# Kernel optimization log

Measured on AMD Instinct MI355X. Metric: run time of the kernel, lower is better.

The kernel has to match this reference:

```python
import jax, jax.numpy as jnp
import numpy as np

POWERS = (0, 1, 2)
IN_F, OUT_F = 64, 64
B, N, T = 8, 2048, 12


def setup_inputs() -> dict:
    key = jax.random.key(0)
    ks = jax.random.split(key, 8)
    inp = {
        "x": jax.random.normal(ks[0], (B, IN_F, N, T), dtype=jnp.float32),
        "adj": jax.random.uniform(ks[1], (B, N, N), dtype=jnp.float32),
    }
    # Xavier-uniform weights per adjacency power, zero biases (as in initialize_weights)
    limit = float(np.sqrt(6.0 / (IN_F + OUT_F)))
    for i, p in enumerate(POWERS):
        inp[f"W{p}"] = jax.random.uniform(ks[2 + i], (IN_F, OUT_F), jnp.float32, -limit, limit)
        inp[f"b{p}"] = jnp.zeros((OUT_F,), jnp.float32)
    return inp


def _gcn_conv(x, adj, W, b, a_power):
    # x: [B, F, N, T]; W: [F, O]; adj: [B, N, N]
    h = jnp.einsum('bfnt,fo->bont', x, W) + b[None, :, None, None]
    # repeated diffusion along node axis: h[f, n] <- sum_m adj[n, m] h[f, m]
    for _ in range(a_power):
        h = jnp.einsum('bnm,bomt->bont', adj, h)
    return jax.nn.leaky_relu(h)  # default negative_slope 0.01, same as torch


def reference(x, adj, W0, b0, W1, b1, W2, b2):
    params = {0: (W0, b0), 1: (W1, b1), 2: (W2, b2)}
    outs = [_gcn_conv(x, adj, params[p][0], params[p][1], p) for p in POWERS]
    return jnp.concatenate(outs, axis=1)  # [B, len(POWERS)*O, N, T]
```

## Files before the change

kernel.cpp:

```cpp
#include <hip/hip_runtime.h>

#define B_ 8
#define N_ 2048
#define T_ 12
#define F_ 64
#define NT 24576
#define CH 192
#define C_ 768

typedef __bf16 bf16x8 __attribute__((ext_vector_type(8)));
typedef float f32x4 __attribute__((ext_vector_type(4)));

typedef const __attribute__((address_space(1))) unsigned int as1_uint;
typedef __attribute__((address_space(3))) unsigned int as3_uint;

__device__ __forceinline__ void gload16(const void* g, void* l) {
  __builtin_amdgcn_global_load_lds((as1_uint*)g, (as3_uint*)l, 16, 0, 0);
}

__device__ __forceinline__ unsigned short f2bf(float f) {
  unsigned int u = __float_as_uint(f);
  u += 0x7FFFu + ((u >> 16) & 1u);
  return (unsigned short)(u >> 16);
}

__device__ __forceinline__ float leaky(float v) {
  return v >= 0.0f ? v : 0.01f * v;
}

__global__ __launch_bounds__(256) void convert_adj_k(const float* __restrict__ adj,
                                                     unsigned short* __restrict__ adjb) {
  size_t i = (size_t)blockIdx.x * 256 + threadIdx.x;
  const float4 v = reinterpret_cast<const float4*>(adj)[i];
  ushort4 u;
  u.x = f2bf(v.x); u.y = f2bf(v.y); u.z = f2bf(v.z); u.w = f2bf(v.w);
  reinterpret_cast<ushort4*>(adjb)[i] = u;
}

__device__ __forceinline__ void stage_wt(const float* __restrict__ W,
                                         unsigned short* Wt, int tid) {
  const int f = tid >> 2;
  const int q = tid & 3;
  const float4* row = reinterpret_cast<const float4*>(W + f * 64 + q * 16);
#pragma unroll
  for (int v4 = 0; v4 < 4; ++v4) {
    float4 v = row[v4];
    const int ob = q * 16 + v4 * 4;
    Wt[(ob + 0) * 72 + f] = f2bf(v.x);
    Wt[(ob + 1) * 72 + f] = f2bf(v.y);
    Wt[(ob + 2) * 72 + f] = f2bf(v.z);
    Wt[(ob + 3) * 72 + f] = f2bf(v.w);
  }
}

__global__ __launch_bounds__(256) void p0_k(const float* __restrict__ x,
                                            const float* __restrict__ W0,
                                            const float* __restrict__ bia0,
                                            float* __restrict__ out) {
  __shared__ unsigned short Wt[64 * 72];
  __shared__ float bias[64];
  const int tid = threadIdx.x;
  stage_wt(W0, Wt, tid);
  if (tid < 64) bias[tid] = bia0[tid];
  __syncthreads();

  const int lane = tid & 63;
  const int wave = tid >> 6;
  const int b = blockIdx.y;
  const int e = blockIdx.x * 64 + wave * 16 + (lane & 15);
  const int fgrp = (lane >> 4) * 8;
  const float* xb = x + (size_t)b * F_ * NT;

  bf16x8 xf[2];
#pragma unroll
  for (int kf = 0; kf < 2; ++kf)
#pragma unroll
    for (int j = 0; j < 8; ++j)
      xf[kf][j] = (__bf16)xb[(size_t)(fgrp + kf * 32 + j) * NT + e];

  float* outb = out + (size_t)b * CH * NT;
#pragma unroll
  for (int ob = 0; ob < 4; ++ob) {
    f32x4 acc = {};
#pragma unroll
    for (int kf = 0; kf < 2; ++kf) {
      bf16x8 af = *reinterpret_cast<const bf16x8*>(
          &Wt[(ob * 16 + (lane & 15)) * 72 + kf * 32 + fgrp]);
      acc = __builtin_amdgcn_mfma_f32_16x16x32_bf16(af, xf[kf], acc, 0, 0, 0);
    }
#pragma unroll
    for (int r = 0; r < 4; ++r) {
      const int o = ob * 16 + (lane >> 4) * 4 + r;
      outb[(size_t)o * NT + e] = leaky(acc[r] + bias[o]);
    }
  }
}

__global__ __launch_bounds__(256) void p12_k(const float* __restrict__ x,
                                             const float* __restrict__ W1,
                                             const float* __restrict__ bia1,
                                             const float* __restrict__ W2,
                                             const float* __restrict__ bia2,
                                             unsigned short* __restrict__ G1,
                                             unsigned short* __restrict__ G2) {
  __shared__ unsigned short Wt[2][64 * 72];
  __shared__ float bias[2][64];
  const int tid = threadIdx.x;
  stage_wt(W1, Wt[0], tid);
  stage_wt(W2, Wt[1], tid);
  if (tid < 64) bias[0][tid] = bia1[tid];
  else if (tid < 128) bias[1][tid - 64] = bia2[tid - 64];
  __syncthreads();

  const int lane = tid & 63;
  const int wave = tid >> 6;
  const int b = blockIdx.y;
  const int n = blockIdx.x * 16 + (lane & 15);
  const int fgrp = (lane >> 4) * 8;
  const float* xb = x + (size_t)b * F_ * NT;
  unsigned short* Gp[2] = {G1 + (size_t)b * C_ * N_, G2 + (size_t)b * C_ * N_};

#pragma unroll
  for (int it = 0; it < 3; ++it) {
    const int t = wave * 3 + it;
    const int e = n * T_ + t;

    bf16x8 xf[2];
#pragma unroll
    for (int kf = 0; kf < 2; ++kf)
#pragma unroll
      for (int j = 0; j < 8; ++j)
        xf[kf][j] = (__bf16)xb[(size_t)(fgrp + kf * 32 + j) * NT + e];

#pragma unroll
    for (int p = 0; p < 2; ++p) {
#pragma unroll
      for (int ob = 0; ob < 4; ++ob) {
        f32x4 acc = {};
#pragma unroll
        for (int kf = 0; kf < 2; ++kf) {
          bf16x8 af = *reinterpret_cast<const bf16x8*>(
              &Wt[p][(ob * 16 + (lane & 15)) * 72 + kf * 32 + fgrp]);
          acc = __builtin_amdgcn_mfma_f32_16x16x32_bf16(af, xf[kf], acc, 0, 0, 0);
        }
#pragma unroll
        for (int r = 0; r < 4; ++r) {
          const int o = ob * 16 + (lane >> 4) * 4 + r;
          Gp[p][(size_t)(o * T_ + t) * N_ + n] = f2bf(acc[r] + bias[p][o]);
        }
      }
    }
  }
}

__global__ __launch_bounds__(512, 2) void gemm8_k(
    const unsigned short* __restrict__ adjb,
    const unsigned short* __restrict__ Bt,
    float* __restrict__ out,
    unsigned short* __restrict__ Ht,
    const int mode, const int ochan_base)
{
  extern __shared__ __align__(16) unsigned short lds[];

  const int tid  = threadIdx.x;
  const int lane = tid & 63;
  const int wave = tid >> 6;
  const int wr = wave >> 2;
  const int wc = wave & 3;

  const int b  = blockIdx.x & 7;
  const int w  = blockIdx.x >> 3;
  const int n0 = (w & 7) * 256;
  const int c0 = (w >> 3) * 192;

  const unsigned short* A  = adjb + (size_t)b * N_ * N_;
  const unsigned short* Bm = Bt   + (size_t)b * C_ * N_;

  const int swzSrc = ((lane & 3) ^ ((lane >> 3) & 3)) * 8;
  const unsigned short* aSt1 = A + (size_t)(n0 + wave * 16 + (lane >> 2)) * N_ + swzSrc;
  const unsigned short* aSt2 = aSt1 + (size_t)128 * N_;
  const unsigned short* bSt1 = Bm + (size_t)(c0 + wave * 16 + (lane >> 2)) * N_ + swzSrc;
  const int brow2 = c0 + 128 + wave * 16 + (lane >> 2);
  const unsigned short* bSt2 = Bm + (size_t)(brow2 < C_ ? brow2 : C_ - 1) * N_ + swzSrc;
  const int ldsW = wave * 512;

  const int kg  = (lane >> 4) ^ ((lane >> 1) & 3);
  const int aRd = (wr * 128 + (lane & 15)) * 32 + kg * 8;
  const int bRd = (wc * 48  + (lane & 15)) * 32 + kg * 8;

  f32x4 acc[8][3] = {};
  bf16x8 afr[8], bfr[3];

#define STGA(LDSB, KT, KH) \
  gload16(aSt1 + (KT) * 64 + (KH) * 32, lds + (LDSB) + (KH) * 8192 + ldsW); \
  gload16(aSt2 + (KT) * 64 + (KH) * 32, lds + (LDSB) + (KH) * 8192 + ldsW + 4096);

#define STGB(LDSB, KT, KH) \
  gload16(bSt1 + (KT) * 64 + (KH) * 32, lds + (LDSB) + (KH) * 8192 + ldsW); \
  gload16(bSt2 + (KT) * 64 + (KH) * 32, lds + (LDSB) + (KH) * 8192 + ldsW + 4096);

#define RD_B(BUFB, KH) { \
  _Pragma("unroll") \
  for (int nf = 0; nf < 3; ++nf) \
    bfr[nf] = *(const bf16x8*)(lds + (BUFB) + (KH) * 8192 + nf * 512 + bRd); }

#define RD_A8(BUFA, KH) { \
  _Pragma("unroll") \
  for (int mm = 0; mm < 8; ++mm) \
    afr[mm] = *(const bf16x8*)(lds + (BUFA) + (KH) * 8192 + mm * 512 + aRd); }

#define MFMA24() { \
  _Pragma("unroll") \
  for (int mm = 0; mm < 8; ++mm) \
  _Pragma("unroll") \
  for (int nf = 0; nf < 3; ++nf) \
    acc[mm][nf] = __builtin_amdgcn_mfma_f32_16x16x32_bf16( \
        afr[mm], bfr[nf], acc[mm][nf], 0, 0, 0); }

#define MIDBAR() \
  __builtin_amdgcn_s_barrier(); \
  asm volatile("s_waitcnt lgkmcnt(0)" ::: "memory"); \
  __builtin_amdgcn_sched_barrier(0); \
  __builtin_amdgcn_s_setprio(1);

#define ENDBAR() \
  __builtin_amdgcn_s_setprio(0); \
  __builtin_amdgcn_s_barrier();

#define WAITV(N) asm volatile("s_waitcnt vmcnt(" #N ")" ::: "memory");

  STGA(0, 0, 0)      STGB(32768, 0, 0)
  STGA(0, 0, 1)      STGB(32768, 0, 1)
  STGA(16384, 1, 0)  STGB(49152, 1, 0)
  WAITV(8)
  __builtin_amdgcn_s_barrier();

#pragma unroll 1
  for (int it = 0; it < 15; ++it) {
    const int kt0 = 2 * it;
    RD_B(32768, 0) RD_A8(0, 0)
    STGA(16384, kt0 + 1, 1) STGB(49152, kt0 + 1, 1)
    WAITV(8)
    MIDBAR() MFMA24() ENDBAR()
    RD_B(32768, 1) RD_A8(0, 1)
    STGA(0, kt0 + 2, 0) STGB(32768, kt0 + 2, 0)
    WAITV(8)
    MIDBAR() MFMA24() ENDBAR()
    RD_B(49152, 0) RD_A8(16384, 0)
    STGA(0, kt0 + 2, 1) STGB(32768, kt0 + 2, 1)
    WAITV(8)
    MIDBAR() MFMA24() ENDBAR()
    RD_B(49152, 1) RD_A8(16384, 1)
    STGA(16384, kt0 + 3, 0) STGB(49152, kt0 + 3, 0)
    WAITV(8)
    MIDBAR() MFMA24() ENDBAR()
  }

  {
    RD_B(32768, 0) RD_A8(0, 0)
    STGA(16384, 31, 1) STGB(49152, 31, 1)
    WAITV(8)
    MIDBAR() MFMA24() ENDBAR()
    RD_B(32768, 1) RD_A8(0, 1)
    WAITV(4)
    MIDBAR() MFMA24() ENDBAR()
    RD_B(49152, 0) RD_A8(16384, 0)
    WAITV(0)
    MIDBAR() MFMA24() ENDBAR()
    RD_B(49152, 1) RD_A8(16384, 1)
    MIDBAR() MFMA24() ENDBAR()
  }

  const int r4 = (lane >> 4) * 4;
  if (mode == 0) {
    float* outb = out + (size_t)b * CH * NT;
#pragma unroll
    for (int m = 0; m < 8; ++m) {
#pragma unroll
      for (int nf = 0; nf < 3; ++nf) {
        const int c = c0 + wc * 48 + nf * 16 + (lane & 15);
        const int o = c / 12;
        const int t = c - o * 12;
#pragma unroll
        for (int r = 0; r < 4; ++r) {
          const int n = n0 + wr * 128 + m * 16 + r4 + r;
          outb[((size_t)(ochan_base + o) * N_ + n) * T_ + t] = leaky(acc[m][nf][r]);
        }
      }
    }
  } else {
    unsigned short* Hb = Ht + (size_t)b * C_ * N_;
#pragma unroll
    for (int m = 0; m < 8; ++m) {
#pragma unroll
      for (int nf = 0; nf < 3; ++nf) {
        const int c = c0 + wc * 48 + nf * 16 + (lane & 15);
        const int nb = n0 + wr * 128 + m * 16 + r4;
        ushort4 u;
        u.x = f2bf(acc[m][nf][0]);
        u.y = f2bf(acc[m][nf][1]);
        u.z = f2bf(acc[m][nf][2]);
        u.w = f2bf(acc[m][nf][3]);
        *reinterpret_cast<ushort4*>(&Hb[(size_t)c * N_ + nb]) = u;
      }
    }
  }
#undef STGA
#undef STGB
#undef RD_B
#undef RD_A8
#undef MFMA24
#undef MIDBAR
#undef ENDBAR
#undef WAITV
}

extern "C" void kernel_launch(void* const* d_in, const int* in_sizes, int n_in,
                              void* d_out, int out_size, void* d_ws, size_t ws_size,
                              hipStream_t stream) {
  const float* x   = (const float*)d_in[0];
  const float* adj = (const float*)d_in[1];
  const float* W0  = (const float*)d_in[2];
  const float* b0  = (const float*)d_in[3];
  const float* W1  = (const float*)d_in[4];
  const float* b1  = (const float*)d_in[5];
  const float* W2  = (const float*)d_in[6];
  const float* b2  = (const float*)d_in[7];
  float* out = (float*)d_out;

  char* ws = (char*)d_ws;
  unsigned short* adjb = (unsigned short*)ws;
  unsigned short* G1   = (unsigned short*)(ws + 67108864);
  unsigned short* G2   = (unsigned short*)(ws + 92274688);
  unsigned short* Ht   = G1;

  hipFuncSetAttribute((const void*)gemm8_k,
                      hipFuncAttributeMaxDynamicSharedMemorySize, 131072);

  hipLaunchKernelGGL(convert_adj_k, dim3((B_ * N_ * N_ / 4) / 256), dim3(256), 0, stream,
                     adj, adjb);

  hipLaunchKernelGGL(p0_k, dim3(NT / 64, B_), dim3(256), 0, stream,
                     x, W0, b0, out);

  hipLaunchKernelGGL(p12_k, dim3(N_ / 16, B_), dim3(256), 0, stream,
                     x, W1, b1, W2, b2, G1, G2);

  hipLaunchKernelGGL(gemm8_k, dim3(256), dim3(512), 131072, stream,
                     adjb, G1, out, (unsigned short*)nullptr, 0, 64);

  hipLaunchKernelGGL(gemm8_k, dim3(256), dim3(512), 131072, stream,
                     adjb, G2, out, Ht, 1, 0);

  hipLaunchKernelGGL(gemm8_k, dim3(256), dim3(512), 131072, stream,
                     adjb, Ht, out, (unsigned short*)nullptr, 0, 128);
}
```

Baseline: 279.6 us.

## Double-buffer LDS fragment registers to overlap next-phase reads with MFMAs

Splits the A/B register fragments into two sets, so each phase issues the LDS reads for the next half-tile while the MFMAs run on the current set. The explicit lgkmcnt(0) wait before the MFMA block is removed, which hides LDS read latency behind matrix work. The cost is 11 more bf16x8 registers per lane on top of a 96-register accumulator. That may raise VGPR pressure or occupancy limits and depends on the compiler inserting correct LDS waits.

```diff
diff --git a/kernel.cpp b/kernel.cpp
--- a/kernel.cpp
+++ b/kernel.cpp
@@ -189,7 +189,7 @@
   const int bRd = (wc * 48  + (lane & 15)) * 32 + kg * 8;
 
   f32x4 acc[8][3] = {};
-  bf16x8 afr[8], bfr[3];
+  bf16x8 afr0[8], afr1[8], bfr0[3], bfr1[3];
 
 #define STGA(LDSB, KT, KH) \
   gload16(aSt1 + (KT) * 64 + (KH) * 32, lds + (LDSB) + (KH) * 8192 + ldsW); \
@@ -199,77 +199,71 @@
   gload16(bSt1 + (KT) * 64 + (KH) * 32, lds + (LDSB) + (KH) * 8192 + ldsW); \
   gload16(bSt2 + (KT) * 64 + (KH) * 32, lds + (LDSB) + (KH) * 8192 + ldsW + 4096);
 
-#define RD_B(BUFB, KH) { \
+#define RD_B(SET, BUFB, KH) { \
   _Pragma("unroll") \
   for (int nf = 0; nf < 3; ++nf) \
-    bfr[nf] = *(const bf16x8*)(lds + (BUFB) + (KH) * 8192 + nf * 512 + bRd); }
-
-#define RD_A8(BUFA, KH) { \
+    bfr##SET[nf] = *(const bf16x8*)(lds + (BUFB) + (KH) * 8192 + nf * 512 + bRd); }
+
+#define RD_A8(SET, BUFA, KH) { \
   _Pragma("unroll") \
   for (int mm = 0; mm < 8; ++mm) \
-    afr[mm] = *(const bf16x8*)(lds + (BUFA) + (KH) * 8192 + mm * 512 + aRd); }
-
-#define MFMA24() { \
+    afr##SET[mm] = *(const bf16x8*)(lds + (BUFA) + (KH) * 8192 + mm * 512 + aRd); }
+
+#define MFMA24(SET) { \
   _Pragma("unroll") \
   for (int mm = 0; mm < 8; ++mm) \
   _Pragma("unroll") \
   for (int nf = 0; nf < 3; ++nf) \
     acc[mm][nf] = __builtin_amdgcn_mfma_f32_16x16x32_bf16( \
-        afr[mm], bfr[nf], acc[mm][nf], 0, 0, 0); }
-
-#define MIDBAR() \
+        afr##SET[mm], bfr##SET[nf], acc[mm][nf], 0, 0, 0); }
+
+#define WAITV_(N) asm volatile("s_waitcnt vmcnt(" #N ")" ::: "memory");
+#define WAITV(N) WAITV_(N)
+
+#define PHASE(SETC, SETN, BUFN, KHN, STBUF, STKT, STKH) \
+  STGA(STBUF, STKT, STKH) STGB((STBUF) + 32768, STKT, STKH) \
+  WAITV(8) \
   __builtin_amdgcn_s_barrier(); \
-  asm volatile("s_waitcnt lgkmcnt(0)" ::: "memory"); \
+  RD_B(SETN, (BUFN) + 32768, KHN) RD_A8(SETN, BUFN, KHN) \
   __builtin_amdgcn_sched_barrier(0); \
-  __builtin_amdgcn_s_setprio(1);
-
-#define ENDBAR() \
+  __builtin_amdgcn_s_setprio(1); \
+  MFMA24(SETC) \
   __builtin_amdgcn_s_setprio(0); \
   __builtin_amdgcn_s_barrier();
 
-#define WAITV(N) asm volatile("s_waitcnt vmcnt(" #N ")" ::: "memory");
+#define PHASE_NOST(SETC, SETN, BUFN, KHN, WVN) \
+  WAITV(WVN) \
+  __builtin_amdgcn_s_barrier(); \
+  RD_B(SETN, (BUFN) + 32768, KHN) RD_A8(SETN, BUFN, KHN) \
+  __builtin_amdgcn_sched_barrier(0); \
+  __builtin_amdgcn_s_setprio(1); \
+  MFMA24(SETC) \
+  __builtin_amdgcn_s_setprio(0); \
+  __builtin_amdgcn_s_barrier();
 
   STGA(0, 0, 0)      STGB(32768, 0, 0)
   STGA(0, 0, 1)      STGB(32768, 0, 1)
   STGA(16384, 1, 0)  STGB(49152, 1, 0)
   WAITV(8)
   __builtin_amdgcn_s_barrier();
+  RD_B(0, 32768, 0) RD_A8(0, 0, 0)
 
 #pragma unroll 1
   for (int it = 0; it < 15; ++it) {
-    const int kt0 = 2 * it;
-    RD_B(32768, 0) RD_A8(0, 0)
-    STGA(16384, kt0 + 1, 1) STGB(49152, kt0 + 1, 1)
-    WAITV(8)
-    MIDBAR() MFMA24() ENDBAR()
-    RD_B(32768, 1) RD_A8(0, 1)
-    STGA(0, kt0 + 2, 0) STGB(32768, kt0 + 2, 0)
-    WAITV(8)
-    MIDBAR() MFMA24() ENDBAR()
-    RD_B(49152, 0) RD_A8(16384, 0)
-    STGA(0, kt0 + 2, 1) STGB(32768, kt0 + 2, 1)
-    WAITV(8)
-    MIDBAR() MFMA24() ENDBAR()
-    RD_B(49152, 1) RD_A8(16384, 1)
-    STGA(16384, kt0 + 3, 0) STGB(49152, kt0 + 3, 0)
-    WAITV(8)
-    MIDBAR() MFMA24() ENDBAR()
-  }
-
-  {
-    RD_B(32768, 0) RD_A8(0, 0)
-    STGA(16384, 31, 1) STGB(49152, 31, 1)
-    WAITV(8)
-    MIDBAR() MFMA24() ENDBAR()
-    RD_B(32768, 1) RD_A8(0, 1)
-    WAITV(4)
-    MIDBAR() MFMA24() ENDBAR()
-    RD_B(49152, 0) RD_A8(16384, 0)
-    WAITV(0)
-    MIDBAR() MFMA24() ENDBAR()
-    RD_B(49152, 1) RD_A8(16384, 1)
-    MIDBAR() MFMA24() ENDBAR()
-  }
+    const int kt2 = 2 * it;
+    PHASE(0, 1, 0, 1, 16384, kt2 + 1, 1)
+    PHASE(1, 0, 16384, 0, 0, kt2 + 2, 0)
+    PHASE(0, 1, 16384, 1, 0, kt2 + 2, 1)
+    PHASE(1, 0, 0, 0, 16384, kt2 + 3, 0)
+  }
+
+  PHASE(0, 1, 0, 1, 16384, 31, 1)
+  PHASE_NOST(1, 0, 16384, 0, 4)
+  PHASE_NOST(0, 1, 16384, 1, 0)
+  __builtin_amdgcn_s_barrier();
+  __builtin_amdgcn_s_setprio(1);
+  MFMA24(1)
+  __builtin_amdgcn_s_setprio(0);
 
   const int r4 = (lane >> 4) * 4;
   if (mode == 0) {
@@ -310,9 +304,10 @@
 #undef RD_B
 #undef RD_A8
 #undef MFMA24
-#undef MIDBAR
-#undef ENDBAR
+#undef PHASE
+#undef PHASE_NOST
 #undef WAITV
+#undef WAITV_
 }
 
 extern "C" void kernel_launch(void* const* d_in, const int* in_sizes, int n_in,
```

Measured after the change: 282.2 us. No clear change (+0.9%).
